# Kernel tuning notes

Measured on AMD Instinct MI355X. Metric: run time of the kernel, lower is better.

The kernel has to match this reference:

```python
import jax, jax.numpy as jnp
import numpy as np

B, T, D, H = 2, 2048, 768, 12
HS = D // H


def setup_inputs() -> dict:
    key = jax.random.key(0)
    ks = jax.random.split(key, 11)
    s = 1.0 / np.sqrt(D)
    return {
        "query": jax.random.normal(ks[0], (B, T, D), jnp.float32),
        "key": jax.random.normal(ks[1], (B, T, D), jnp.float32),
        "value": jax.random.normal(ks[2], (B, T, D), jnp.float32),
        "Wq": jax.random.normal(ks[3], (D, D), jnp.float32) * s,
        "bq": jax.random.normal(ks[4], (D,), jnp.float32) * s,
        "Wk": jax.random.normal(ks[5], (D, D), jnp.float32) * s,
        "bk": jax.random.normal(ks[6], (D,), jnp.float32) * s,
        "Wv": jax.random.normal(ks[7], (D, D), jnp.float32) * s,
        "bv": jax.random.normal(ks[8], (D,), jnp.float32) * s,
        "Wo": jax.random.normal(ks[9], (D, D), jnp.float32) * s,
        "bo": jax.random.normal(ks[10], (D,), jnp.float32) * s,
    }


def reference(query, key, value, Wq, bq, Wk, bk, Wv, bv, Wo, bo):
    # Projections (torch nn.Linear: x @ W.T + b), then split heads -> [B,H,T,HS]
    def split_heads(x):
        return x.reshape(B, -1, H, HS).transpose(0, 2, 1, 3)

    q = split_heads(query @ Wq.T + bq)
    k = split_heads(key @ Wk.T + bk)
    v = split_heads(value @ Wv.T + bv)

    scale = 1.0 / jnp.sqrt(jnp.asarray(HS, q.dtype))
    scores = jnp.einsum("bhqd,bhkd->bhqk", q, k) * scale  # [B,H,Tq,Tk]
    attn = jax.nn.softmax(scores, axis=-1)
    out = jnp.einsum("bhqk,bhkd->bhqd", attn, v)  # [B,H,Tq,HS]
    out = out.transpose(0, 2, 1, 3).reshape(B, -1, D)
    output = out @ Wo.T + bo
    return output, attn.mean(axis=1)
```

## Files before the change

### kernel.cpp

```cpp
#include <hip/hip_runtime.h>
#include <hip/hip_fp16.h>
#include <stdint.h>

typedef _Float16 f16;
typedef _Float16 f16x8 __attribute__((ext_vector_type(8)));
typedef _Float16 f16x4v __attribute__((ext_vector_type(4)));
typedef __fp16 h16x2 __attribute__((ext_vector_type(2)));
typedef float f32x4 __attribute__((ext_vector_type(4)));

#define MFMA16(a,b,c) __builtin_amdgcn_mfma_f32_16x16x32_f16(a,b,c,0,0,0)
#define CVTPK(a,b) __builtin_amdgcn_cvt_pkrtz(a,b)

#if __has_builtin(__builtin_amdgcn_exp2f)
#define EXP2(x) __builtin_amdgcn_exp2f(x)
#else
#define EXP2(x) exp2f(x)
#endif

static __device__ __forceinline__ float dot2acc(h16x2 a, float c) {
#if __has_builtin(__builtin_amdgcn_fdot2)
    const h16x2 one = { (__fp16)1.f, (__fp16)1.f };
    return __builtin_amdgcn_fdot2(a, one, c, false);
#else
    return c + (float)a[0] + (float)a[1];
#endif
}

typedef __attribute__((address_space(1))) void gvoid_t;
typedef __attribute__((address_space(3))) void svoid_t;
#define AS1(p) ((gvoid_t*)(uintptr_t)(p))
#define AS3(p) ((svoid_t*)(uint32_t)(uintptr_t)(p))

static constexpr int Bc = 2, Tc = 2048, Dc = 768, Hc = 12;
static constexpr int Mc = Bc * Tc;
static constexpr float SC2 = 0.18033688011112042f;

union PA { f16x8 v; h16x2 h[4]; };

#define FRAG(BASE, ROW16, HALF) \
    (*(const f16x8*)((const char*)(BASE) + \
        (((((ROW16) + lg) * 8) + ((((HALF) * 4 + hg)) ^ (lg & 7))) * 16)))

__global__ __launch_bounds__(256) void conv_all(
    const float* __restrict__ q, const float* __restrict__ k, const float* __restrict__ v,
    const float* __restrict__ wq, const float* __restrict__ wk, const float* __restrict__ wv,
    const float* __restrict__ wo,
    f16* __restrict__ qh, f16* __restrict__ kh, f16* __restrict__ vh,
    f16* __restrict__ wqh, f16* __restrict__ wkh, f16* __restrict__ wvh, f16* __restrict__ woh)
{
    const int NI = (Mc * Dc) / 4;
    const int NW = (Dc * Dc) / 4;
    int i = blockIdx.x * 256 + threadIdx.x;
    if (i >= 3 * NI + 4 * NW) return;
    const float4* src; f16* dst; int j; float scl = 1.f;
    if (i < 3 * NI) {
        int a = i / NI; j = i - a * NI;
        src = (const float4*)(a == 0 ? q : (a == 1 ? k : v));
        dst = (a == 0 ? qh : (a == 1 ? kh : vh));
    } else {
        int t = i - 3 * NI;
        int a = t / NW; j = t - a * NW;
        src = (const float4*)(a == 0 ? wq : (a == 1 ? wk : (a == 2 ? wv : wo)));
        dst = (a == 0 ? wqh : (a == 1 ? wkh : (a == 2 ? wvh : woh)));
        if (a == 0) scl = SC2;
    }
    float4 f = src[j];
    f16x4v o = { (f16)(f.x * scl), (f16)(f.y * scl), (f16)(f.z * scl), (f16)(f.w * scl) };
    *(f16x4v*)(dst + 4 * j) = o;
}

__device__ __forceinline__ void gemm_tile_mainloop(
    const f16* __restrict__ A, const f16* __restrict__ W,
    int brow, int bcol, f16* As, f16* Bs, f32x4 acc[4][4])
{
    const int tid = threadIdx.x;
    const int w = tid >> 6, lane = tid & 63;
    const int lg = lane & 15, hg = lane >> 4;
    const int wr = w >> 1, wc = w & 1;

    for (int kt = 0; kt < 768 / 32; ++kt) {
        const int k0 = kt * 32;
#pragma unroll
        for (int j = 0; j < 2; ++j) {
            int p = (w * 2 + j) * 1024 + lane * 16;
            int r = p >> 6;
            int ke = (p & 63) >> 1;
            __builtin_amdgcn_global_load_lds(AS1(A + (size_t)(brow + r) * 768 + k0 + ke),
                                             AS3((char*)As + (w * 2 + j) * 1024), 16, 0, 0);
            __builtin_amdgcn_global_load_lds(AS1(W + (size_t)(bcol + r) * 768 + k0 + ke),
                                             AS3((char*)Bs + (w * 2 + j) * 1024), 16, 0, 0);
        }
        __syncthreads();
        f16x8 af[4], bf[4];
#pragma unroll
        for (int m = 0; m < 4; ++m)
            af[m] = *(const f16x8*)(As + (wr * 64 + m * 16 + lg) * 32 + hg * 8);
#pragma unroll
        for (int n = 0; n < 4; ++n)
            bf[n] = *(const f16x8*)(Bs + (wc * 64 + n * 16 + lg) * 32 + hg * 8);
#pragma unroll
        for (int m = 0; m < 4; ++m)
#pragma unroll
            for (int n = 0; n < 4; ++n)
                acc[m][n] = MFMA16(af[m], bf[n], acc[m][n]);
        __syncthreads();
    }
}

__global__ __launch_bounds__(256) void qkv_proj(
    const f16* __restrict__ qh, const f16* __restrict__ kh, const f16* __restrict__ vh,
    const f16* __restrict__ wqh, const f16* __restrict__ wkh, const f16* __restrict__ wvh,
    const float* __restrict__ bq, const float* __restrict__ bk, const float* __restrict__ bv,
    f16* __restrict__ Qp, f16* __restrict__ Kp, f16* __restrict__ Vt)
{
    __shared__ f16 As[128 * 32], Bs[128 * 32];
    const int z = blockIdx.z;
    const f16* A = (z == 0) ? qh : (z == 1) ? kh : vh;
    const f16* W = (z == 0) ? wqh : (z == 1) ? wkh : wvh;
    const float* bias = (z == 0) ? bq : (z == 1) ? bk : bv;
    const int brow = blockIdx.y * 128, bcol = blockIdx.x * 128;

    f32x4 acc[4][4];
    const f32x4 z4 = { 0.f, 0.f, 0.f, 0.f };
#pragma unroll
    for (int m = 0; m < 4; ++m)
#pragma unroll
        for (int n = 0; n < 4; ++n) acc[m][n] = z4;

    gemm_tile_mainloop(A, W, brow, bcol, As, Bs, acc);

    const int tid = threadIdx.x, w = tid >> 6, lane = tid & 63;
    const int lg = lane & 15, hg = lane >> 4, wr = w >> 1, wc = w & 1;
#pragma unroll
    for (int n = 0; n < 4; ++n) {
        const int c = bcol + wc * 64 + n * 16 + lg;
        const float bval = (z == 0) ? bias[c] * SC2 : bias[c];
#pragma unroll
        for (int m = 0; m < 4; ++m) {
            const int r0 = brow + wr * 64 + m * 16 + hg * 4;
#pragma unroll
            for (int r = 0; r < 4; ++r) {
                const float val = acc[m][n][r] + bval;
                const int row = r0 + r;
                if (z == 0) {
                    Qp[(size_t)row * 768 + c] = (f16)val;
                } else if (z == 1) {
                    Kp[(size_t)row * 768 + c] = (f16)val;
                } else {
                    const int bb = row >> 11, t = row & 2047;
                    const int hh = c >> 6, d = c & 63;
                    const int j = t & 15, cc = (t >> 4) & 1;
                    const int tp = (t & ~31) | ((j >> 2) * 8 + cc * 4 + (j & 3));
                    Vt[(((size_t)(bb * 12 + hh)) * 64 + d) * 2048 + tp] = (f16)val;
                }
            }
        }
    }
}

__global__ __launch_bounds__(256) void out_proj(
    const f16* __restrict__ ctx, const f16* __restrict__ woh,
    const float* __restrict__ bo, float* __restrict__ out)
{
    __shared__ f16 As[128 * 32], Bs[128 * 32];
    const int brow = blockIdx.y * 128, bcol = blockIdx.x * 128;
    f32x4 acc[4][4];
    const f32x4 z4 = { 0.f, 0.f, 0.f, 0.f };
#pragma unroll
    for (int m = 0; m < 4; ++m)
#pragma unroll
        for (int n = 0; n < 4; ++n) acc[m][n] = z4;

    gemm_tile_mainloop(ctx, woh, brow, bcol, As, Bs, acc);

    const int tid = threadIdx.x, w = tid >> 6, lane = tid & 63;
    const int lg = lane & 15, hg = lane >> 4, wr = w >> 1, wc = w & 1;
#pragma unroll
    for (int n = 0; n < 4; ++n) {
        const int c = bcol + wc * 64 + n * 16 + lg;
        const float bval = bo[c];
#pragma unroll
        for (int m = 0; m < 4; ++m) {
            const int r0 = brow + wr * 64 + m * 16 + hg * 4;
#pragma unroll
            for (int r = 0; r < 4; ++r)
                out[(size_t)(r0 + r) * 768 + c] = acc[m][n][r] + bval;
        }
    }
}

__global__ __launch_bounds__(256) void attn_out(
    const f16* __restrict__ Qp, const f16* __restrict__ Kp, const f16* __restrict__ Vt,
    float* __restrict__ l_inv, f16* __restrict__ ctx)
{
    __shared__ f16 Kbuf[2][4096];
    __shared__ f16 Vbuf[2][4096];

    const int qt = blockIdx.x, h = blockIdx.y, b = blockIdx.z;
    const int tid = threadIdx.x, w = tid >> 6, lane = tid & 63;
    const int lg = lane & 15, hg = lane >> 4;
    const int wbase16 = (tid & ~63) * 16;

    const size_t qrow0 = (size_t)b * 2048 + qt * 64 + w * 16;
    const int hcol = h * 64;
    const f16* qbase = Qp + (qrow0 + lg) * 768 + hcol + hg * 8;
    const f16x8 bq0 = *(const f16x8*)(qbase);
    const f16x8 bq1 = *(const f16x8*)(qbase + 32);

    const size_t kbase = (size_t)b * 2048;
    const f16* Vg = Vt + ((size_t)(b * 12 + h)) * 64 * 2048;

    const f32x4 z4 = { 0.f, 0.f, 0.f, 0.f };
    f32x4 oacc[4];
#pragma unroll
    for (int n = 0; n < 4; ++n) oacc[n] = z4;
    float lsum = 0.f;

#define STAGE_KV(KT_, BUF) do { \
    _Pragma("unroll") \
    for (int j_ = 0; j_ < 2; ++j_) { \
        const int p_ = j_ * 256 + tid; \
        const int row_ = p_ >> 3, c_ = (p_ & 7) ^ (row_ & 7); \
        __builtin_amdgcn_global_load_lds( \
            AS1(Kp + (kbase + (size_t)(KT_) * 64 + row_) * 768 + hcol + c_ * 8), \
            AS3((char*)&Kbuf[BUF][0] + j_ * 4096 + wbase16), 16, 0, 0); \
        __builtin_amdgcn_global_load_lds( \
            AS1(Vg + (size_t)row_ * 2048 + (KT_) * 64 + c_ * 8), \
            AS3((char*)&Vbuf[BUF][0] + j_ * 4096 + wbase16), 16, 0, 0); \
    } } while (0)

#define AOBODY(CUR) do { \
    const f16* Kb_ = &Kbuf[CUR][0]; const f16* Vb_ = &Vbuf[CUR][0]; \
    f32x4 sa0 = z4, sa1 = z4, sa2 = z4, sa3 = z4; \
    sa0 = MFMA16(FRAG(Kb_, 0,  0), bq0, sa0); sa0 = MFMA16(FRAG(Kb_, 0,  1), bq1, sa0); \
    sa1 = MFMA16(FRAG(Kb_, 16, 0), bq0, sa1); sa1 = MFMA16(FRAG(Kb_, 16, 1), bq1, sa1); \
    sa2 = MFMA16(FRAG(Kb_, 32, 0), bq0, sa2); sa2 = MFMA16(FRAG(Kb_, 32, 1), bq1, sa2); \
    sa3 = MFMA16(FRAG(Kb_, 48, 0), bq0, sa3); sa3 = MFMA16(FRAG(Kb_, 48, 1), bq1, sa3); \
    const float p0  = EXP2(sa0[0]), p1  = EXP2(sa0[1]); \
    const float p2  = EXP2(sa0[2]), p3  = EXP2(sa0[3]); \
    const float p4  = EXP2(sa1[0]), p5  = EXP2(sa1[1]); \
    const float p6  = EXP2(sa1[2]), p7  = EXP2(sa1[3]); \
    const float p8  = EXP2(sa2[0]), p9  = EXP2(sa2[1]); \
    const float p10 = EXP2(sa2[2]), p11 = EXP2(sa2[3]); \
    const float p12 = EXP2(sa3[0]), p13 = EXP2(sa3[1]); \
    const float p14 = EXP2(sa3[2]), p15 = EXP2(sa3[3]); \
    PA pa0, pa1; \
    pa0.h[0] = CVTPK(p0, p1);   pa0.h[1] = CVTPK(p2, p3); \
    pa0.h[2] = CVTPK(p4, p5);   pa0.h[3] = CVTPK(p6, p7); \
    pa1.h[0] = CVTPK(p8, p9);   pa1.h[1] = CVTPK(p10, p11); \
    pa1.h[2] = CVTPK(p12, p13); pa1.h[3] = CVTPK(p14, p15); \
    float t0_ = 0.f, t1_ = 0.f; \
    t0_ = dot2acc(pa0.h[0], t0_); t0_ = dot2acc(pa0.h[1], t0_); \
    t0_ = dot2acc(pa0.h[2], t0_); t0_ = dot2acc(pa0.h[3], t0_); \
    t1_ = dot2acc(pa1.h[0], t1_); t1_ = dot2acc(pa1.h[1], t1_); \
    t1_ = dot2acc(pa1.h[2], t1_); t1_ = dot2acc(pa1.h[3], t1_); \
    lsum += t0_ + t1_; \
    oacc[0] = MFMA16(pa0.v, FRAG(Vb_, 0,  0), oacc[0]); oacc[0] = MFMA16(pa1.v, FRAG(Vb_, 0,  1), oacc[0]); \
    oacc[1] = MFMA16(pa0.v, FRAG(Vb_, 16, 0), oacc[1]); oacc[1] = MFMA16(pa1.v, FRAG(Vb_, 16, 1), oacc[1]); \
    oacc[2] = MFMA16(pa0.v, FRAG(Vb_, 32, 0), oacc[2]); oacc[2] = MFMA16(pa1.v, FRAG(Vb_, 32, 1), oacc[2]); \
    oacc[3] = MFMA16(pa0.v, FRAG(Vb_, 48, 0), oacc[3]); oacc[3] = MFMA16(pa1.v, FRAG(Vb_, 48, 1), oacc[3]); \
} while (0)

    STAGE_KV(0, 0);
    __syncthreads();
    for (int kt = 0; kt < 32; ++kt) {
        const int cur = kt & 1;
        if (kt < 31) STAGE_KV(kt + 1, cur ^ 1);
        AOBODY(cur);
        __syncthreads();
    }
#undef STAGE_KV
#undef AOBODY

    lsum += __shfl_xor(lsum, 16);
    lsum += __shfl_xor(lsum, 32);
    const float iv = 1.f / lsum;
    if (hg == 0)
        l_inv[((size_t)(b * 12 + h)) * 2048 + qt * 64 + w * 16 + lg] = iv;
    float ivr[4];
#pragma unroll
    for (int r = 0; r < 4; ++r) ivr[r] = __shfl(iv, hg * 4 + r);
#pragma unroll
    for (int n = 0; n < 4; ++n)
#pragma unroll
        for (int r = 0; r < 4; ++r)
            ctx[(qrow0 + hg * 4 + r) * 768 + hcol + n * 16 + lg] = (f16)(oacc[n][r] * ivr[r]);
}

__global__ __launch_bounds__(256) void attn_mean(
    const f16* __restrict__ Qp, const f16* __restrict__ Kp,
    const float* __restrict__ l_inv, float* __restrict__ om)
{
    __shared__ f16 Qbuf[2][4096];
    __shared__ f16 Kbuf[2][4096];

    const int kt = blockIdx.x, qt = blockIdx.y, b = blockIdx.z;
    const int tid = threadIdx.x, w = tid >> 6, lane = tid & 63;
    const int lg = lane & 15, hg = lane >> 4;
    const int wbase16 = (tid & ~63) * 16;
    const size_t qrow0 = (size_t)b * 2048 + qt * 64 + w * 16;
    const size_t qtrow = (size_t)b * 2048 + qt * 64;
    const size_t ktrow = (size_t)b * 2048 + kt * 64;

    float macc[4][4];
#pragma unroll
    for (int n = 0; n < 4; ++n)
#pragma unroll
        for (int r = 0; r < 4; ++r) macc[n][r] = 0.f;

    const f32x4 z4 = { 0.f, 0.f, 0.f, 0.f };

#define STAGE_QK(H_, BUF) do { \
    _Pragma("unroll") \
    for (int j_ = 0; j_ < 2; ++j_) { \
        const int p_ = j_ * 256 + tid; \
        const int row_ = p_ >> 3, c_ = (p_ & 7) ^ (row_ & 7); \
        __builtin_amdgcn_global_load_lds( \
            AS1(Qp + (qtrow + row_) * 768 + (H_) * 64 + c_ * 8), \
            AS3((char*)&Qbuf[BUF][0] + j_ * 4096 + wbase16), 16, 0, 0); \
        __builtin_amdgcn_global_load_lds( \
            AS1(Kp + (ktrow + row_) * 768 + (H_) * 64 + c_ * 8), \
            AS3((char*)&Kbuf[BUF][0] + j_ * 4096 + wbase16), 16, 0, 0); \
    } } while (0)

#define MBODY(H_, CUR) do { \
    const f16* Qb_ = &Qbuf[CUR][0]; const f16* Kb_ = &Kbuf[CUR][0]; \
    const f16x8 q0_ = FRAG(Qb_, w * 16, 0), q1_ = FRAG(Qb_, w * 16, 1); \
    f32x4 sa0 = z4, sa1 = z4, sa2 = z4, sa3 = z4; \
    sa0 = MFMA16(q0_, FRAG(Kb_, 0,  0), sa0); sa0 = MFMA16(q1_, FRAG(Kb_, 0,  1), sa0); \
    sa1 = MFMA16(q0_, FRAG(Kb_, 16, 0), sa1); sa1 = MFMA16(q1_, FRAG(Kb_, 16, 1), sa1); \
    sa2 = MFMA16(q0_, FRAG(Kb_, 32, 0), sa2); sa2 = MFMA16(q1_, FRAG(Kb_, 32, 1), sa2); \
    sa3 = MFMA16(q0_, FRAG(Kb_, 48, 0), sa3); sa3 = MFMA16(q1_, FRAG(Kb_, 48, 1), sa3); \
    const float4 iv_ = *(const float4*)(l_inv + ((size_t)(b * 12 + (H_))) * 2048 \
                                        + qt * 64 + w * 16 + hg * 4); \
    _Pragma("unroll") \
    for (int r_ = 0; r_ < 4; ++r_) { \
        const float ivv = ((const float*)&iv_)[r_]; \
        macc[0][r_] += EXP2(sa0[r_]) * ivv; \
        macc[1][r_] += EXP2(sa1[r_]) * ivv; \
        macc[2][r_] += EXP2(sa2[r_]) * ivv; \
        macc[3][r_] += EXP2(sa3[r_]) * ivv; } \
} while (0)

    STAGE_QK(0, 0);
    __syncthreads();
    for (int h = 0; h < 12; ++h) {
        const int cur = h & 1;
        if (h < 11) STAGE_QK(h + 1, cur ^ 1);
        MBODY(h, cur);
        __syncthreads();
    }
#undef STAGE_QK
#undef MBODY

#pragma unroll
    for (int n = 0; n < 4; ++n)
#pragma unroll
        for (int r = 0; r < 4; ++r) {
            const size_t row = qrow0 + hg * 4 + r;
            const size_t col = (size_t)kt * 64 + n * 16 + lg;
            om[row * 2048 + col] = macc[n][r] * (1.0f / 12.0f);
        }
}

extern "C" void kernel_launch(void* const* d_in, const int* in_sizes, int n_in,
                              void* d_out, int out_size, void* d_ws, size_t ws_size,
                              hipStream_t stream) {
    const float* q  = (const float*)d_in[0];
    const float* k  = (const float*)d_in[1];
    const float* v  = (const float*)d_in[2];
    const float* Wq = (const float*)d_in[3];
    const float* bq = (const float*)d_in[4];
    const float* Wk = (const float*)d_in[5];
    const float* bk = (const float*)d_in[6];
    const float* Wv = (const float*)d_in[7];
    const float* bv = (const float*)d_in[8];
    const float* Wo = (const float*)d_in[9];
    const float* bo = (const float*)d_in[10];
    float* out = (float*)d_out;

    char* ws = (char*)d_ws;
    const size_t SZ_IN = (size_t)Mc * Dc * 2;
    const size_t SZ_W  = (size_t)Dc * Dc * 2;
    f16* qh  = (f16*)(ws);
    f16* kh  = (f16*)(ws + SZ_IN);
    f16* vh  = (f16*)(ws + 2 * SZ_IN);
    f16* wqh = (f16*)(ws + 3 * SZ_IN);
    f16* wkh = (f16*)(ws + 3 * SZ_IN + SZ_W);
    f16* wvh = (f16*)(ws + 3 * SZ_IN + 2 * SZ_W);
    f16* woh = (f16*)(ws + 3 * SZ_IN + 3 * SZ_W);
    f16* Qp  = (f16*)(ws + 3 * SZ_IN + 4 * SZ_W);
    f16* Kp  = (f16*)(ws + 4 * SZ_IN + 4 * SZ_W);
    f16* Vt  = (f16*)(ws + 5 * SZ_IN + 4 * SZ_W);
    f16* ctx = qh;
    float* l_inv = (float*)kh;

    conv_all<<<dim3(11520), dim3(256), 0, stream>>>(q, k, v, Wq, Wk, Wv, Wo,
                                                    qh, kh, vh, wqh, wkh, wvh, woh);
    qkv_proj<<<dim3(6, 32, 3), dim3(256), 0, stream>>>(qh, kh, vh, wqh, wkh, wvh,
                                                       bq, bk, bv, Qp, Kp, Vt);
    attn_out<<<dim3(32, 12, 2), dim3(256), 0, stream>>>(Qp, Kp, Vt, l_inv, ctx);
    attn_mean<<<dim3(32, 32, 2), dim3(256), 0, stream>>>(Qp, Kp, l_inv,
                                                         out + (size_t)Mc * Dc);
    out_proj<<<dim3(6, 32, 1), dim3(256), 0, stream>>>(ctx, woh, bo, out);
}
```

Before: 145.9 us.

## Switch attention kernels to 32x32x16 MFMA with split-K reduction and new V swizzle

Both attention kernels move from 16x16x32 to 32x32x16 MFMA tiles. In attn_out each wave now owns 32 query rows and half of each 64-key tile, and the two key halves are combined through shared memory at the end. attn_mean drops to 128 threads per block with 32x32 output tiles per wave and float4 stores. The V transpose swizzle in qkv_proj changes to match the new fragment layout. The larger MFMA tiles are meant to cut LDS fragment traffic and instruction count, in exchange for more registers, extra LDS for the reduction and different occupancy from the new launch bounds.

Result: no change. 145.2 us (-0.4%).

```diff
diff --git a/kernel.cpp b/kernel.cpp
--- a/kernel.cpp
+++ b/kernel.cpp
@@ -7,8 +7,10 @@
 typedef _Float16 f16x4v __attribute__((ext_vector_type(4)));
 typedef __fp16 h16x2 __attribute__((ext_vector_type(2)));
 typedef float f32x4 __attribute__((ext_vector_type(4)));
+typedef float f32x16 __attribute__((ext_vector_type(16)));
 
 #define MFMA16(a,b,c) __builtin_amdgcn_mfma_f32_16x16x32_f16(a,b,c,0,0,0)
+#define MFMA32(a,b,c) __builtin_amdgcn_mfma_f32_32x32x16_f16(a,b,c,0,0,0)
 #define CVTPK(a,b) __builtin_amdgcn_cvt_pkrtz(a,b)
 
 #if __has_builtin(__builtin_amdgcn_exp2f)
@@ -37,9 +39,9 @@
 
 union PA { f16x8 v; h16x2 h[4]; };
 
-#define FRAG(BASE, ROW16, HALF) \
+#define FRAG32(BASE, ROWOFF, CHUNK) \
     (*(const f16x8*)((const char*)(BASE) + \
-        (((((ROW16) + lg) * 8) + ((((HALF) * 4 + hg)) ^ (lg & 7))) * 16)))
+        ((ROWOFF) + q32) * 128 + (((CHUNK) ^ g7) * 16)))
 
 __global__ __launch_bounds__(256) void conv_all(
     const float* __restrict__ q, const float* __restrict__ k, const float* __restrict__ v,
@@ -149,8 +151,9 @@
                 } else {
                     const int bb = row >> 11, t = row & 2047;
                     const int hh = c >> 6, d = c & 63;
-                    const int j = t & 15, cc = (t >> 4) & 1;
-                    const int tp = (t & ~31) | ((j >> 2) * 8 + cc * 4 + (j & 3));
+                    const int tl = t & 31;
+                    const int sw = ((tl >> 2) ^ (tl >> 3)) & 1;
+                    const int tp = (t & ~31) | (tl ^ (sw * 12));
                     Vt[(((size_t)(bb * 12 + hh)) * 64 + d) * 2048 + tp] = (f16)val;
                 }
             }
@@ -189,31 +192,37 @@
     }
 }
 
-__global__ __launch_bounds__(256) void attn_out(
+__global__ __launch_bounds__(256, 3) void attn_out(
     const f16* __restrict__ Qp, const f16* __restrict__ Kp, const f16* __restrict__ Vt,
     float* __restrict__ l_inv, f16* __restrict__ ctx)
 {
     __shared__ f16 Kbuf[2][4096];
     __shared__ f16 Vbuf[2][4096];
+    __shared__ float Ored[2][32][64];
+    __shared__ float lred[2][2][32];
 
     const int qt = blockIdx.x, h = blockIdx.y, b = blockIdx.z;
     const int tid = threadIdx.x, w = tid >> 6, lane = tid & 63;
-    const int lg = lane & 15, hg = lane >> 4;
+    const int q32 = lane & 31, hi = lane >> 5, g7 = lane & 7;
+    const int qh = w & 1, kh = w >> 1;
     const int wbase16 = (tid & ~63) * 16;
 
-    const size_t qrow0 = (size_t)b * 2048 + qt * 64 + w * 16;
+    const size_t qrow0 = (size_t)b * 2048 + qt * 64 + qh * 32;
     const int hcol = h * 64;
-    const f16* qbase = Qp + (qrow0 + lg) * 768 + hcol + hg * 8;
-    const f16x8 bq0 = *(const f16x8*)(qbase);
-    const f16x8 bq1 = *(const f16x8*)(qbase + 32);
+
+    const f16* qb = Qp + (qrow0 + q32) * 768 + hcol + hi * 8;
+    f16x8 bqf[4];
+#pragma unroll
+    for (int d = 0; d < 4; ++d) bqf[d] = *(const f16x8*)(qb + d * 16);
 
     const size_t kbase = (size_t)b * 2048;
     const f16* Vg = Vt + ((size_t)(b * 12 + h)) * 64 * 2048;
 
-    const f32x4 z4 = { 0.f, 0.f, 0.f, 0.f };
-    f32x4 oacc[4];
-#pragma unroll
-    for (int n = 0; n < 4; ++n) oacc[n] = z4;
+    f32x16 oacc[2];
+#pragma unroll
+    for (int dt = 0; dt < 2; ++dt)
+#pragma unroll
+        for (int r = 0; r < 16; ++r) oacc[dt][r] = 0.f;
     float lsum = 0.f;
 
 #define STAGE_KV(KT_, BUF) do { \
@@ -231,34 +240,31 @@
 
 #define AOBODY(CUR) do { \
     const f16* Kb_ = &Kbuf[CUR][0]; const f16* Vb_ = &Vbuf[CUR][0]; \
-    f32x4 sa0 = z4, sa1 = z4, sa2 = z4, sa3 = z4; \
-    sa0 = MFMA16(FRAG(Kb_, 0,  0), bq0, sa0); sa0 = MFMA16(FRAG(Kb_, 0,  1), bq1, sa0); \
-    sa1 = MFMA16(FRAG(Kb_, 16, 0), bq0, sa1); sa1 = MFMA16(FRAG(Kb_, 16, 1), bq1, sa1); \
-    sa2 = MFMA16(FRAG(Kb_, 32, 0), bq0, sa2); sa2 = MFMA16(FRAG(Kb_, 32, 1), bq1, sa2); \
-    sa3 = MFMA16(FRAG(Kb_, 48, 0), bq0, sa3); sa3 = MFMA16(FRAG(Kb_, 48, 1), bq1, sa3); \
-    const float p0  = EXP2(sa0[0]), p1  = EXP2(sa0[1]); \
-    const float p2  = EXP2(sa0[2]), p3  = EXP2(sa0[3]); \
-    const float p4  = EXP2(sa1[0]), p5  = EXP2(sa1[1]); \
-    const float p6  = EXP2(sa1[2]), p7  = EXP2(sa1[3]); \
-    const float p8  = EXP2(sa2[0]), p9  = EXP2(sa2[1]); \
-    const float p10 = EXP2(sa2[2]), p11 = EXP2(sa2[3]); \
-    const float p12 = EXP2(sa3[0]), p13 = EXP2(sa3[1]); \
-    const float p14 = EXP2(sa3[2]), p15 = EXP2(sa3[3]); \
+    f32x16 sa; \
+    _Pragma("unroll") \
+    for (int r_ = 0; r_ < 16; ++r_) sa[r_] = 0.f; \
+    sa = MFMA32(FRAG32(Kb_, kh * 32, 0 + hi), bqf[0], sa); \
+    sa = MFMA32(FRAG32(Kb_, kh * 32, 2 + hi), bqf[1], sa); \
+    sa = MFMA32(FRAG32(Kb_, kh * 32, 4 + hi), bqf[2], sa); \
+    sa = MFMA32(FRAG32(Kb_, kh * 32, 6 + hi), bqf[3], sa); \
+    float p[16]; \
+    _Pragma("unroll") \
+    for (int r_ = 0; r_ < 16; ++r_) p[r_] = EXP2(sa[r_]); \
     PA pa0, pa1; \
-    pa0.h[0] = CVTPK(p0, p1);   pa0.h[1] = CVTPK(p2, p3); \
-    pa0.h[2] = CVTPK(p4, p5);   pa0.h[3] = CVTPK(p6, p7); \
-    pa1.h[0] = CVTPK(p8, p9);   pa1.h[1] = CVTPK(p10, p11); \
-    pa1.h[2] = CVTPK(p12, p13); pa1.h[3] = CVTPK(p14, p15); \
+    pa0.h[0] = CVTPK(p[0], p[1]);   pa0.h[1] = CVTPK(p[2], p[3]); \
+    pa0.h[2] = CVTPK(p[4], p[5]);   pa0.h[3] = CVTPK(p[6], p[7]); \
+    pa1.h[0] = CVTPK(p[8], p[9]);   pa1.h[1] = CVTPK(p[10], p[11]); \
+    pa1.h[2] = CVTPK(p[12], p[13]); pa1.h[3] = CVTPK(p[14], p[15]); \
     float t0_ = 0.f, t1_ = 0.f; \
     t0_ = dot2acc(pa0.h[0], t0_); t0_ = dot2acc(pa0.h[1], t0_); \
     t0_ = dot2acc(pa0.h[2], t0_); t0_ = dot2acc(pa0.h[3], t0_); \
     t1_ = dot2acc(pa1.h[0], t1_); t1_ = dot2acc(pa1.h[1], t1_); \
     t1_ = dot2acc(pa1.h[2], t1_); t1_ = dot2acc(pa1.h[3], t1_); \
     lsum += t0_ + t1_; \
-    oacc[0] = MFMA16(pa0.v, FRAG(Vb_, 0,  0), oacc[0]); oacc[0] = MFMA16(pa1.v, FRAG(Vb_, 0,  1), oacc[0]); \
-    oacc[1] = MFMA16(pa0.v, FRAG(Vb_, 16, 0), oacc[1]); oacc[1] = MFMA16(pa1.v, FRAG(Vb_, 16, 1), oacc[1]); \
-    oacc[2] = MFMA16(pa0.v, FRAG(Vb_, 32, 0), oacc[2]); oacc[2] = MFMA16(pa1.v, FRAG(Vb_, 32, 1), oacc[2]); \
-    oacc[3] = MFMA16(pa0.v, FRAG(Vb_, 48, 0), oacc[3]); oacc[3] = MFMA16(pa1.v, FRAG(Vb_, 48, 1), oacc[3]); \
+    oacc[0] = MFMA32(FRAG32(Vb_, 0,  kh * 4 + 0 + hi), pa0.v, oacc[0]); \
+    oacc[0] = MFMA32(FRAG32(Vb_, 0,  kh * 4 + 2 + hi), pa1.v, oacc[0]); \
+    oacc[1] = MFMA32(FRAG32(Vb_, 32, kh * 4 + 0 + hi), pa0.v, oacc[1]); \
+    oacc[1] = MFMA32(FRAG32(Vb_, 32, kh * 4 + 2 + hi), pa1.v, oacc[1]); \
 } while (0)
 
     STAGE_KV(0, 0);
@@ -272,22 +278,40 @@
 #undef STAGE_KV
 #undef AOBODY
 
-    lsum += __shfl_xor(lsum, 16);
     lsum += __shfl_xor(lsum, 32);
-    const float iv = 1.f / lsum;
-    if (hg == 0)
-        l_inv[((size_t)(b * 12 + h)) * 2048 + qt * 64 + w * 16 + lg] = iv;
-    float ivr[4];
-#pragma unroll
-    for (int r = 0; r < 4; ++r) ivr[r] = __shfl(iv, hg * 4 + r);
-#pragma unroll
-    for (int n = 0; n < 4; ++n)
-#pragma unroll
-        for (int r = 0; r < 4; ++r)
-            ctx[(qrow0 + hg * 4 + r) * 768 + hcol + n * 16 + lg] = (f16)(oacc[n][r] * ivr[r]);
-}
-
-__global__ __launch_bounds__(256) void attn_mean(
+    if (hi == 0) lred[kh][qh][q32] = lsum;
+    if (kh == 1) {
+#pragma unroll
+        for (int dt = 0; dt < 2; ++dt)
+#pragma unroll
+            for (int g = 0; g < 4; ++g) {
+                float4 v4 = { oacc[dt][g * 4 + 0], oacc[dt][g * 4 + 1],
+                              oacc[dt][g * 4 + 2], oacc[dt][g * 4 + 3] };
+                *(float4*)&Ored[qh][q32][dt * 32 + g * 8 + hi * 4] = v4;
+            }
+    }
+    __syncthreads();
+    if (kh == 0) {
+        const float iv = 1.f / (lred[0][qh][q32] + lred[1][qh][q32]);
+        if (hi == 0)
+            l_inv[((size_t)(b * 12 + h)) * 2048 + qt * 64 + qh * 32 + q32] = iv;
+        f16* cb = ctx + (qrow0 + q32) * 768 + hcol;
+#pragma unroll
+        for (int dt = 0; dt < 2; ++dt)
+#pragma unroll
+            for (int g = 0; g < 4; ++g) {
+                const int d0 = dt * 32 + g * 8 + hi * 4;
+                const float4 o4 = *(const float4*)&Ored[qh][q32][d0];
+                f16x4v s;
+#pragma unroll
+                for (int e = 0; e < 4; ++e)
+                    s[e] = (f16)((oacc[dt][g * 4 + e] + (&o4.x)[e]) * iv);
+                *(f16x4v*)(cb + d0) = s;
+            }
+    }
+}
+
+__global__ __launch_bounds__(128, 2) void attn_mean(
     const f16* __restrict__ Qp, const f16* __restrict__ Kp,
     const float* __restrict__ l_inv, float* __restrict__ om)
 {
@@ -295,51 +319,54 @@
     __shared__ f16 Kbuf[2][4096];
 
     const int kt = blockIdx.x, qt = blockIdx.y, b = blockIdx.z;
-    const int tid = threadIdx.x, w = tid >> 6, lane = tid & 63;
-    const int lg = lane & 15, hg = lane >> 4;
-    const int wbase16 = (tid & ~63) * 16;
-    const size_t qrow0 = (size_t)b * 2048 + qt * 64 + w * 16;
+    const int tid = threadIdx.x, lane = tid & 63;
+    const int q32 = lane & 31, hi = lane >> 5, g7 = lane & 7;
+    const int qh = tid >> 6;
+    const int wb = (tid & 64) * 16;
+
     const size_t qtrow = (size_t)b * 2048 + qt * 64;
     const size_t ktrow = (size_t)b * 2048 + kt * 64;
 
-    float macc[4][4];
-#pragma unroll
-    for (int n = 0; n < 4; ++n)
-#pragma unroll
-        for (int r = 0; r < 4; ++r) macc[n][r] = 0.f;
-
-    const f32x4 z4 = { 0.f, 0.f, 0.f, 0.f };
+    f32x16 macc[2];
+#pragma unroll
+    for (int kk = 0; kk < 2; ++kk)
+#pragma unroll
+        for (int r = 0; r < 16; ++r) macc[kk][r] = 0.f;
 
 #define STAGE_QK(H_, BUF) do { \
     _Pragma("unroll") \
-    for (int j_ = 0; j_ < 2; ++j_) { \
-        const int p_ = j_ * 256 + tid; \
+    for (int j_ = 0; j_ < 4; ++j_) { \
+        const int p_ = j_ * 128 + tid; \
         const int row_ = p_ >> 3, c_ = (p_ & 7) ^ (row_ & 7); \
         __builtin_amdgcn_global_load_lds( \
             AS1(Qp + (qtrow + row_) * 768 + (H_) * 64 + c_ * 8), \
-            AS3((char*)&Qbuf[BUF][0] + j_ * 4096 + wbase16), 16, 0, 0); \
+            AS3((char*)&Qbuf[BUF][0] + j_ * 2048 + wb), 16, 0, 0); \
         __builtin_amdgcn_global_load_lds( \
             AS1(Kp + (ktrow + row_) * 768 + (H_) * 64 + c_ * 8), \
-            AS3((char*)&Kbuf[BUF][0] + j_ * 4096 + wbase16), 16, 0, 0); \
+            AS3((char*)&Kbuf[BUF][0] + j_ * 2048 + wb), 16, 0, 0); \
     } } while (0)
 
 #define MBODY(H_, CUR) do { \
     const f16* Qb_ = &Qbuf[CUR][0]; const f16* Kb_ = &Kbuf[CUR][0]; \
-    const f16x8 q0_ = FRAG(Qb_, w * 16, 0), q1_ = FRAG(Qb_, w * 16, 1); \
-    f32x4 sa0 = z4, sa1 = z4, sa2 = z4, sa3 = z4; \
-    sa0 = MFMA16(q0_, FRAG(Kb_, 0,  0), sa0); sa0 = MFMA16(q1_, FRAG(Kb_, 0,  1), sa0); \
-    sa1 = MFMA16(q0_, FRAG(Kb_, 16, 0), sa1); sa1 = MFMA16(q1_, FRAG(Kb_, 16, 1), sa1); \
-    sa2 = MFMA16(q0_, FRAG(Kb_, 32, 0), sa2); sa2 = MFMA16(q1_, FRAG(Kb_, 32, 1), sa2); \
-    sa3 = MFMA16(q0_, FRAG(Kb_, 48, 0), sa3); sa3 = MFMA16(q1_, FRAG(Kb_, 48, 1), sa3); \
-    const float4 iv_ = *(const float4*)(l_inv + ((size_t)(b * 12 + (H_))) * 2048 \
-                                        + qt * 64 + w * 16 + hg * 4); \
-    _Pragma("unroll") \
-    for (int r_ = 0; r_ < 4; ++r_) { \
-        const float ivv = ((const float*)&iv_)[r_]; \
+    f16x8 qf[4]; \
+    _Pragma("unroll") \
+    for (int d_ = 0; d_ < 4; ++d_) qf[d_] = FRAG32(Qb_, qh * 32, d_ * 2 + hi); \
+    f32x16 sa0, sa1; \
+    _Pragma("unroll") \
+    for (int r_ = 0; r_ < 16; ++r_) { sa0[r_] = 0.f; sa1[r_] = 0.f; } \
+    sa0 = MFMA32(FRAG32(Kb_, 0,  0 + hi), qf[0], sa0); \
+    sa0 = MFMA32(FRAG32(Kb_, 0,  2 + hi), qf[1], sa0); \
+    sa0 = MFMA32(FRAG32(Kb_, 0,  4 + hi), qf[2], sa0); \
+    sa0 = MFMA32(FRAG32(Kb_, 0,  6 + hi), qf[3], sa0); \
+    sa1 = MFMA32(FRAG32(Kb_, 32, 0 + hi), qf[0], sa1); \
+    sa1 = MFMA32(FRAG32(Kb_, 32, 2 + hi), qf[1], sa1); \
+    sa1 = MFMA32(FRAG32(Kb_, 32, 4 + hi), qf[2], sa1); \
+    sa1 = MFMA32(FRAG32(Kb_, 32, 6 + hi), qf[3], sa1); \
+    const float ivv = l_inv[((size_t)(b * 12 + (H_))) * 2048 + qt * 64 + qh * 32 + q32]; \
+    _Pragma("unroll") \
+    for (int r_ = 0; r_ < 16; ++r_) { \
         macc[0][r_] += EXP2(sa0[r_]) * ivv; \
-        macc[1][r_] += EXP2(sa1[r_]) * ivv; \
-        macc[2][r_] += EXP2(sa2[r_]) * ivv; \
-        macc[3][r_] += EXP2(sa3[r_]) * ivv; } \
+        macc[1][r_] += EXP2(sa1[r_]) * ivv; } \
 } while (0)
 
     STAGE_QK(0, 0);
@@ -353,13 +380,16 @@
 #undef STAGE_QK
 #undef MBODY
 
-#pragma unroll
-    for (int n = 0; n < 4; ++n)
-#pragma unroll
-        for (int r = 0; r < 4; ++r) {
-            const size_t row = qrow0 + hg * 4 + r;
-            const size_t col = (size_t)kt * 64 + n * 16 + lg;
-            om[row * 2048 + col] = macc[n][r] * (1.0f / 12.0f);
+    float* ob = om + ((size_t)(b * 2048 + qt * 64 + qh * 32 + q32)) * 2048 + kt * 64;
+#pragma unroll
+    for (int kk = 0; kk < 2; ++kk)
+#pragma unroll
+        for (int g = 0; g < 4; ++g) {
+            float4 v4 = { macc[kk][g * 4 + 0] * (1.0f / 12.0f),
+                          macc[kk][g * 4 + 1] * (1.0f / 12.0f),
+                          macc[kk][g * 4 + 2] * (1.0f / 12.0f),
+                          macc[kk][g * 4 + 3] * (1.0f / 12.0f) };
+            *(float4*)(ob + kk * 32 + g * 8 + hi * 4) = v4;
         }
 }
 
@@ -400,7 +430,7 @@
     qkv_proj<<<dim3(6, 32, 3), dim3(256), 0, stream>>>(qh, kh, vh, wqh, wkh, wvh,
                                                        bq, bk, bv, Qp, Kp, Vt);
     attn_out<<<dim3(32, 12, 2), dim3(256), 0, stream>>>(Qp, Kp, Vt, l_inv, ctx);
-    attn_mean<<<dim3(32, 32, 2), dim3(256), 0, stream>>>(Qp, Kp, l_inv,
+    attn_mean<<<dim3(32, 32, 2), dim3(128), 0, stream>>>(Qp, Kp, l_inv,
                                                          out + (size_t)Mc * Dc);
     out_proj<<<dim3(6, 32, 1), dim3(256), 0, stream>>>(ctx, woh, bo, out);
 }
```
